# Performance work log

Measured on AMD Instinct MI355X. Metric: run time of the kernel, lower is better.

## Reference

```python
import jax, jax.numpy as jnp
import numpy as np

NEG_SLOPE = 0.01  # torch nn.LeakyReLU default


def setup_inputs() -> dict:
    key = jax.random.key(0)
    ks = jax.random.split(key, 6)
    B, L, C, D = 4, 1024, 128, 64
    return {
        "queries": jax.random.normal(ks[0], (B, L, C), dtype=jnp.float32),
        "keys": jax.random.normal(ks[1], (B, L, C), dtype=jnp.float32),
        "values": jax.random.normal(ks[2], (B, L, C), dtype=jnp.float32),
        "linear_l": jax.random.normal(ks[3], (C, D), dtype=jnp.float32) * 0.05,
        "linear_r": jax.random.normal(ks[4], (C, D), dtype=jnp.float32) * 0.05,
        "a": jax.random.normal(ks[5], (D, 1), dtype=jnp.float32) * 0.05,
    }


def reference(queries, keys, values, linear_l, linear_r, a):
    # keys/values are accepted by the torch forward but unused in its math.
    # g_l, g_r: (B, L, D)
    g_l = jnp.einsum('blc,cd->bld', queries, linear_l)
    g_r = jnp.einsum('blc,cd->bld', queries, linear_r)
    # torch repeat/repeat_interleave + view(b,l,l,-1) yields
    # g_sum[b, x, y] = g_l[b, y] + g_r[b, x]  -> (B, L, L, D)
    g_sum = g_l[:, None, :, :] + g_r[:, :, None, :]
    g_sum = jnp.where(g_sum >= 0, g_sum, NEG_SLOPE * g_sum)  # LeakyReLU
    e = jnp.einsum('bxyd,d->bxy', g_sum, a[:, 0])            # (B, L, L)
    scores = jax.nn.softmax(e, axis=-1)                       # dropout is identity in eval
    y = jnp.einsum('bxy,byd->bxd', scores, g_r)               # (B, L, D)
    return (y, scores)
```

## Files before the change

kernel.cpp:

```cpp
#include <hip/hip_runtime.h>
#include <math.h>

#define LL   1024
#define NROW 4096
#define DD   64
#define CC   128

#define C1H 0.505f
#define C2H 0.495f

typedef short    bf16x8 __attribute__((ext_vector_type(8)));
typedef float    f32x4  __attribute__((ext_vector_type(4)));
typedef _Float16 hf2    __attribute__((ext_vector_type(2)));

#if defined(__has_builtin)
#if __has_builtin(__builtin_amdgcn_fdot2)
#define HAS_FDOT2 1
#endif
#endif

static __device__ __forceinline__ unsigned short bf16rne(float f) {
  unsigned u = __float_as_uint(f);
  u += 0x7fffu + ((u >> 16) & 1u);
  return (unsigned short)(u >> 16);
}

static __device__ __forceinline__ unsigned rflu(unsigned v) {
  return __builtin_amdgcn_readfirstlane(v);
}
static __device__ __forceinline__ float rflf(float v) {
  return __uint_as_float(__builtin_amdgcn_readfirstlane(__float_as_uint(v)));
}

static __device__ __forceinline__ float dot2abs(unsigned glp, unsigned grp,
                                                unsigned ap, float acc) {
  union { unsigned u; hf2 h; } g1, g2, z, av;
  g1.u = glp; g2.u = grp; av.u = ap;
  z.h = g1.h + g2.h;
  z.u &= 0x7fff7fffu;
#ifdef HAS_FDOT2
  return __builtin_amdgcn_fdot2(z.h, av.h, acc, false);
#else
  return fmaf((float)z.h.y, (float)av.h.y,
              fmaf((float)z.h.x, (float)av.h.x, acc));
#endif
}

__global__ __launch_bounds__(256) void k_proj(
    const float* __restrict__ q, const float* __restrict__ Wl,
    const float* __restrict__ Wr, const float* __restrict__ a,
    uint4* __restrict__ glg, _Float16* __restrict__ gr16,
    unsigned short* __restrict__ grT_bf,
    float* __restrict__ AL, float* __restrict__ AR) {
  const int bl0 = blockIdx.x * 8;
  const int b = bl0 >> 10;
  const int t = threadIdx.x;
  __shared__ __align__(16) float qs[8 * CC];
  __shared__ __align__(16) unsigned short trT[DD][8];
  __shared__ __align__(16) _Float16 trL[8][DD];

  ((float4*)qs)[t] = ((const float4*)(q + (size_t)bl0 * CC))[t];
  __syncthreads();

  const int rr = t >> 6;
  const int d  = t & 63;
  const int r0 = rr * 2, r1 = rr * 2 + 1;
  const float* q0 = qs + r0 * CC;
  const float* q1 = qs + r1 * CC;

  float aL0 = 0, aL1 = 0, aR0 = 0, aR1 = 0;
  float bL0 = 0, bL1 = 0, bR0 = 0, bR1 = 0;
#pragma unroll 8
  for (int c = 0; c < CC; c += 2) {
    float wl0 = Wl[c * DD + d],       wr0 = Wr[c * DD + d];
    float wl1 = Wl[(c + 1) * DD + d], wr1 = Wr[(c + 1) * DD + d];
    aL0 = fmaf(q0[c], wl0, aL0);  bL0 = fmaf(q0[c + 1], wl1, bL0);
    aL1 = fmaf(q1[c], wl0, aL1);  bL1 = fmaf(q1[c + 1], wl1, bL1);
    aR0 = fmaf(q0[c], wr0, aR0);  bR0 = fmaf(q0[c + 1], wr1, bR0);
    aR1 = fmaf(q1[c], wr0, aR1);  bR1 = fmaf(q1[c + 1], wr1, bR1);
  }
  float gL0 = aL0 + bL0, gL1 = aL1 + bL1;
  float gR0 = aR0 + bR0, gR1 = aR1 + bR1;

  trL[r0][d] = (_Float16)gL0;
  trL[r1][d] = (_Float16)gL1;
  gr16[(size_t)(bl0 + r0) * DD + d] = (_Float16)gR0;
  gr16[(size_t)(bl0 + r1) * DD + d] = (_Float16)gR1;
  trT[d][r0] = bf16rne(gR0);
  trT[d][r1] = bf16rne(gR1);

  float av = a[d];
  float vL0 = av * gL0, vL1 = av * gL1, vR0 = av * gR0, vR1 = av * gR1;
#pragma unroll
  for (int off = 1; off < 64; off <<= 1) {
    vL0 += __shfl_xor(vL0, off, 64);
    vL1 += __shfl_xor(vL1, off, 64);
    vR0 += __shfl_xor(vR0, off, 64);
    vR1 += __shfl_xor(vR1, off, 64);
  }
  if (d == 0) {
    AL[bl0 + r0] = vL0; AL[bl0 + r1] = vL1;
    AR[bl0 + r0] = vR0; AR[bl0 + r1] = vR1;
  }
  __syncthreads();
  if (t < 64) {
    *(uint4*)&grT_bf[(((size_t)(b * 64 + t)) << 10) + (bl0 & 1023)] =
        *(const uint4*)&trT[t][0];
  } else if (t < 128) {
    int tt = t - 64;
    int r = tt >> 3, g = tt & 7;
    glg[(((size_t)(b * 8 + g)) << 10) + (bl0 & 1023) + r] =
        *(const uint4*)&trL[r][g * 8];
  }
}

__global__ __launch_bounds__(512, 4) void k_fused(
    const uint4* __restrict__ glg, const _Float16* __restrict__ gr16,
    const unsigned short* __restrict__ grT_bf,
    const float* __restrict__ AL, const float* __restrict__ AR,
    const float* __restrict__ a,
    float* __restrict__ scores, float* __restrict__ yout) {
  const int bl0 = blockIdx.x * 8;
  const int b = bl0 >> 10;
  const int t = threadIdx.x;
  const int w = t >> 6, l = t & 63;

  __shared__ __align__(16) _Float16 grL[8 * DD];
  __shared__ __align__(16) unsigned short eb[8704];
  __shared__ __align__(16) float sPV[8][4][8][17];
  __shared__ __align__(16) float sMx[8][8];
  __shared__ __align__(16) float sSx[8][8];

  uint4 gv[4][2][2];
#pragma unroll
  for (int dblk = 0; dblk < 4; ++dblk)
#pragma unroll
    for (int yc = 0; yc < 2; ++yc)
#pragma unroll
      for (int g2 = 0; g2 < 2; ++g2)
        gv[dblk][yc][g2] =
            glg[(((size_t)(b * 8 + dblk * 2 + g2)) << 10) + yc * 512 + t];

  if (t < 256)
    ((unsigned*)grL)[t] = ((const unsigned*)(gr16 + (size_t)bl0 * DD))[t];

  unsigned sa[32];
#pragma unroll
  for (int k = 0; k < 16; ++k) {
    float4 av = *(const float4*)&a[k * 4];
    union { hf2 h; unsigned u; } u0, u1;
    u0.h.x = (_Float16)av.x; u0.h.y = (_Float16)av.y;
    u1.h.x = (_Float16)av.z; u1.h.y = (_Float16)av.w;
    sa[k * 2]     = rflu(u0.u);
    sa[k * 2 + 1] = rflu(u1.u);
  }

  float pr[8];
#pragma unroll
  for (int x = 0; x < 8; ++x) pr[x] = C1H * rflf(AR[bl0 + x]);

  float alv[2];
  alv[0] = AL[b * LL + t];
  alv[1] = AL[b * LL + 512 + t];

  float pacc[8][2];
#pragma unroll
  for (int x = 0; x < 8; ++x) { pacc[x][0] = 0.f; pacc[x][1] = 0.f; }

  __syncthreads();

#pragma unroll
  for (int dblk = 0; dblk < 4; ++dblk) {
#pragma unroll
    for (int x = 0; x < 8; ++x) {
      uint4 gra = *(const uint4*)&grL[x * DD + dblk * 16];
      uint4 grb = *(const uint4*)&grL[x * DD + dblk * 16 + 8];
#pragma unroll
      for (int yc = 0; yc < 2; ++yc) {
        float s = pacc[x][yc];
        s = dot2abs(gv[dblk][yc][0].x, gra.x, sa[dblk * 8 + 0], s);
        s = dot2abs(gv[dblk][yc][0].y, gra.y, sa[dblk * 8 + 1], s);
        s = dot2abs(gv[dblk][yc][0].z, gra.z, sa[dblk * 8 + 2], s);
        s = dot2abs(gv[dblk][yc][0].w, gra.w, sa[dblk * 8 + 3], s);
        s = dot2abs(gv[dblk][yc][1].x, grb.x, sa[dblk * 8 + 4], s);
        s = dot2abs(gv[dblk][yc][1].y, grb.y, sa[dblk * 8 + 5], s);
        s = dot2abs(gv[dblk][yc][1].z, grb.z, sa[dblk * 8 + 6], s);
        s = dot2abs(gv[dblk][yc][1].w, grb.w, sa[dblk * 8 + 7], s);
        pacc[x][yc] = s;
      }
    }
  }

  float ev[8][2];
#pragma unroll
  for (int x = 0; x < 8; ++x)
#pragma unroll
    for (int yc = 0; yc < 2; ++yc)
      ev[x][yc] = fmaf(C2H, pacc[x][yc], pr[x] + C1H * alv[yc]);

  float lm[8];
#pragma unroll
  for (int x = 0; x < 8; ++x) lm[x] = fmaxf(ev[x][0], ev[x][1]);
#pragma unroll
  for (int off = 1; off < 64; off <<= 1) {
#pragma unroll
    for (int x = 0; x < 8; ++x) lm[x] = fmaxf(lm[x], __shfl_xor(lm[x], off, 64));
  }
  if (l == 0) {
#pragma unroll
    for (int x = 0; x < 8; ++x) sMx[x][w] = lm[x];
  }
  __syncthreads();

  float mfin[8], lsum[8];
#pragma unroll
  for (int x = 0; x < 8; ++x) {
    float4 m0 = *(const float4*)&sMx[x][0];
    float4 m1 = *(const float4*)&sMx[x][4];
    mfin[x] = fmaxf(fmaxf(fmaxf(m0.x, m0.y), fmaxf(m0.z, m0.w)),
                    fmaxf(fmaxf(m1.x, m1.y), fmaxf(m1.z, m1.w)));
  }
#pragma unroll
  for (int x = 0; x < 8; ++x) {
    ev[x][0] = __expf(ev[x][0] - mfin[x]);
    ev[x][1] = __expf(ev[x][1] - mfin[x]);
    lsum[x] = ev[x][0] + ev[x][1];
  }
#pragma unroll
  for (int off = 1; off < 64; off <<= 1) {
#pragma unroll
    for (int x = 0; x < 8; ++x) lsum[x] += __shfl_xor(lsum[x], off, 64);
  }
  if (l == 0) {
#pragma unroll
    for (int x = 0; x < 8; ++x) sSx[x][w] = lsum[x];
  }
  __syncthreads();

  float isv[8];
#pragma unroll
  for (int x = 0; x < 8; ++x) {
    float4 s0 = *(const float4*)&sSx[x][0];
    float4 s1 = *(const float4*)&sSx[x][4];
    isv[x] = 1.0f / (((s0.x + s0.y) + (s0.z + s0.w)) +
                     ((s1.x + s1.y) + (s1.z + s1.w)));
  }

#pragma unroll
  for (int yc = 0; yc < 2; ++yc) {
    int y = yc * 512 + t;
    int kc = y >> 5, k32 = t & 31;
#pragma unroll
    for (int x = 0; x < 8; ++x) {
      float p = ev[x][yc] * isv[x];
      __builtin_nontemporal_store(p, &scores[((size_t)(bl0 + x) << 10) + y]);
      eb[kc * 256 + x * 32 + k32] = bf16rne(p);
    }
  }
  __syncthreads();

  f32x4 acc[4] = {{0.f, 0.f, 0.f, 0.f}, {0.f, 0.f, 0.f, 0.f},
                  {0.f, 0.f, 0.f, 0.f}, {0.f, 0.f, 0.f, 0.f}};
  const int row16 = l & 15, hh = l >> 4;
  const size_t bnBase = ((size_t)b * 64) << 10;
#pragma unroll
  for (int kk = 0; kk < 4; ++kk) {
    int kc = w * 4 + kk;
    bf16x8 af = *(const bf16x8*)&eb[kc * 256 + row16 * 32 + hh * 8];
#pragma unroll
    for (int nt = 0; nt < 4; ++nt) {
      bf16x8 bfv = *(const bf16x8*)(grT_bf + bnBase +
                     (((size_t)(nt * 16 + row16)) << 10) + kc * 32 + hh * 8);
      acc[nt] = __builtin_amdgcn_mfma_f32_16x16x32_bf16(af, bfv, acc[nt], 0, 0, 0);
    }
  }
  if (l < 32) {
#pragma unroll
    for (int nt = 0; nt < 4; ++nt)
#pragma unroll
      for (int i = 0; i < 4; ++i)
        sPV[w][nt][hh * 4 + i][row16] = acc[nt][i];
  }
  __syncthreads();
  {
    int x = t >> 6, dcol = t & 63, nt = dcol >> 4, col = dcol & 15;
    float r = 0.f;
#pragma unroll
    for (int ww = 0; ww < 8; ++ww) r += sPV[ww][nt][x][col];
    yout[(size_t)(bl0 + x) * DD + dcol] = r;
  }
}

extern "C" void kernel_launch(void* const* d_in, const int* in_sizes, int n_in,
                              void* d_out, int out_size, void* d_ws, size_t ws_size,
                              hipStream_t stream) {
  const float* q  = (const float*)d_in[0];
  const float* Wl = (const float*)d_in[3];
  const float* Wr = (const float*)d_in[4];
  const float* a  = (const float*)d_in[5];

  float* yout = (float*)d_out;
  float* esc  = yout + NROW * DD;

  float* ws = (float*)d_ws;
  float* AL = ws;
  float* AR = AL + NROW;
  uint4* glg = (uint4*)(AR + NROW);
  _Float16* gr16 = (_Float16*)(glg + (size_t)NROW * 8);
  unsigned short* grT_bf = (unsigned short*)(gr16 + (size_t)NROW * DD);

  k_proj <<<NROW / 8, 256, 0, stream>>>(q, Wl, Wr, a, glg, gr16, grT_bf, AL, AR);
  k_fused<<<NROW / 8, 512, 0, stream>>>(glg, gr16, grT_bf, AL, AR, a, esc, yout);
}
```

Before: 38.71 us.

## Halve query rows per block and stream key tiles per d-block

Each fused block now handles 4 query rows instead of 8, doubling the grid to 1024 blocks. Key-side gl vectors are loaded per d-block inside the loop rather than all up front, cutting register pressure, and launch bounds now ask for 8 blocks per CU. The bf16 score tile is padded with zeros so the 16-row MFMA tile still works with 4 valid rows. The aim is more parallelism and occupancy. The cost is twice as many reloads of the key-side data and of grT per query row, and half of each MFMA tile's rows are wasted.

```diff
diff --git a/kernel.cpp b/kernel.cpp
--- a/kernel.cpp
+++ b/kernel.cpp
@@ -114,35 +114,29 @@
   }
 }
 
-__global__ __launch_bounds__(512, 4) void k_fused(
+__global__ __launch_bounds__(512, 8) void k_fused(
     const uint4* __restrict__ glg, const _Float16* __restrict__ gr16,
     const unsigned short* __restrict__ grT_bf,
     const float* __restrict__ AL, const float* __restrict__ AR,
     const float* __restrict__ a,
     float* __restrict__ scores, float* __restrict__ yout) {
-  const int bl0 = blockIdx.x * 8;
+  const int bl0 = blockIdx.x * 4;
   const int b = bl0 >> 10;
   const int t = threadIdx.x;
   const int w = t >> 6, l = t & 63;
 
-  __shared__ __align__(16) _Float16 grL[8 * DD];
-  __shared__ __align__(16) unsigned short eb[8704];
-  __shared__ __align__(16) float sPV[8][4][8][17];
-  __shared__ __align__(16) float sMx[8][8];
-  __shared__ __align__(16) float sSx[8][8];
-
-  uint4 gv[4][2][2];
-#pragma unroll
-  for (int dblk = 0; dblk < 4; ++dblk)
-#pragma unroll
-    for (int yc = 0; yc < 2; ++yc)
-#pragma unroll
-      for (int g2 = 0; g2 < 2; ++g2)
-        gv[dblk][yc][g2] =
-            glg[(((size_t)(b * 8 + dblk * 2 + g2)) << 10) + yc * 512 + t];
-
-  if (t < 256)
+  __shared__ __align__(16) _Float16 grL[4 * DD];
+  __shared__ __align__(16) unsigned short eb[4608];
+  __shared__ __align__(16) float sPV[8][4][4][17];
+  __shared__ __align__(16) float sMx[4][8];
+  __shared__ __align__(16) float sSx[4][8];
+
+  if (t < 128)
     ((unsigned*)grL)[t] = ((const unsigned*)(gr16 + (size_t)bl0 * DD))[t];
+  if (t >= 256 && t < 384) {
+    uint2 z = {0u, 0u};
+    ((uint2*)&eb[4096])[t - 256] = z;
+  }
 
   unsigned sa[32];
 #pragma unroll
@@ -155,73 +149,80 @@
     sa[k * 2 + 1] = rflu(u1.u);
   }
 
-  float pr[8];
-#pragma unroll
-  for (int x = 0; x < 8; ++x) pr[x] = C1H * rflf(AR[bl0 + x]);
+  float pr[4];
+#pragma unroll
+  for (int x = 0; x < 4; ++x) pr[x] = C1H * rflf(AR[bl0 + x]);
 
   float alv[2];
   alv[0] = AL[b * LL + t];
   alv[1] = AL[b * LL + 512 + t];
 
-  float pacc[8][2];
-#pragma unroll
-  for (int x = 0; x < 8; ++x) { pacc[x][0] = 0.f; pacc[x][1] = 0.f; }
+  float pacc[4][2];
+#pragma unroll
+  for (int x = 0; x < 4; ++x) { pacc[x][0] = 0.f; pacc[x][1] = 0.f; }
 
   __syncthreads();
 
 #pragma unroll
   for (int dblk = 0; dblk < 4; ++dblk) {
-#pragma unroll
-    for (int x = 0; x < 8; ++x) {
+    uint4 gv[2][2];
+#pragma unroll
+    for (int yc = 0; yc < 2; ++yc)
+#pragma unroll
+      for (int g2 = 0; g2 < 2; ++g2)
+        gv[yc][g2] =
+            glg[(((size_t)(b * 8 + dblk * 2 + g2)) << 10) + yc * 512 + t];
+#pragma unroll
+    for (int x = 0; x < 4; ++x) {
       uint4 gra = *(const uint4*)&grL[x * DD + dblk * 16];
       uint4 grb = *(const uint4*)&grL[x * DD + dblk * 16 + 8];
 #pragma unroll
       for (int yc = 0; yc < 2; ++yc) {
         float s = pacc[x][yc];
-        s = dot2abs(gv[dblk][yc][0].x, gra.x, sa[dblk * 8 + 0], s);
-        s = dot2abs(gv[dblk][yc][0].y, gra.y, sa[dblk * 8 + 1], s);
-        s = dot2abs(gv[dblk][yc][0].z, gra.z, sa[dblk * 8 + 2], s);
-        s = dot2abs(gv[dblk][yc][0].w, gra.w, sa[dblk * 8 + 3], s);
-        s = dot2abs(gv[dblk][yc][1].x, grb.x, sa[dblk * 8 + 4], s);
-        s = dot2abs(gv[dblk][yc][1].y, grb.y, sa[dblk * 8 + 5], s);
-        s = dot2abs(gv[dblk][yc][1].z, grb.z, sa[dblk * 8 + 6], s);
-        s = dot2abs(gv[dblk][yc][1].w, grb.w, sa[dblk * 8 + 7], s);
+        s = dot2abs(gv[yc][0].x, gra.x, sa[dblk * 8 + 0], s);
+        s = dot2abs(gv[yc][0].y, gra.y, sa[dblk * 8 + 1], s);
+        s = dot2abs(gv[yc][0].z, gra.z, sa[dblk * 8 + 2], s);
+        s = dot2abs(gv[yc][0].w, gra.w, sa[dblk * 8 + 3], s);
+        s = dot2abs(gv[yc][1].x, grb.x, sa[dblk * 8 + 4], s);
+        s = dot2abs(gv[yc][1].y, grb.y, sa[dblk * 8 + 5], s);
+        s = dot2abs(gv[yc][1].z, grb.z, sa[dblk * 8 + 6], s);
+        s = dot2abs(gv[yc][1].w, grb.w, sa[dblk * 8 + 7], s);
         pacc[x][yc] = s;
       }
     }
   }
 
-  float ev[8][2];
-#pragma unroll
-  for (int x = 0; x < 8; ++x)
+  float ev[4][2];
+#pragma unroll
+  for (int x = 0; x < 4; ++x)
 #pragma unroll
     for (int yc = 0; yc < 2; ++yc)
       ev[x][yc] = fmaf(C2H, pacc[x][yc], pr[x] + C1H * alv[yc]);
 
-  float lm[8];
-#pragma unroll
-  for (int x = 0; x < 8; ++x) lm[x] = fmaxf(ev[x][0], ev[x][1]);
+  float lm[4];
+#pragma unroll
+  for (int x = 0; x < 4; ++x) lm[x] = fmaxf(ev[x][0], ev[x][1]);
 #pragma unroll
   for (int off = 1; off < 64; off <<= 1) {
 #pragma unroll
-    for (int x = 0; x < 8; ++x) lm[x] = fmaxf(lm[x], __shfl_xor(lm[x], off, 64));
+    for (int x = 0; x < 4; ++x) lm[x] = fmaxf(lm[x], __shfl_xor(lm[x], off, 64));
   }
   if (l == 0) {
 #pragma unroll
-    for (int x = 0; x < 8; ++x) sMx[x][w] = lm[x];
-  }
-  __syncthreads();
-
-  float mfin[8], lsum[8];
-#pragma unroll
-  for (int x = 0; x < 8; ++x) {
+    for (int x = 0; x < 4; ++x) sMx[x][w] = lm[x];
+  }
+  __syncthreads();
+
+  float mfin[4], lsum[4];
+#pragma unroll
+  for (int x = 0; x < 4; ++x) {
     float4 m0 = *(const float4*)&sMx[x][0];
     float4 m1 = *(const float4*)&sMx[x][4];
     mfin[x] = fmaxf(fmaxf(fmaxf(m0.x, m0.y), fmaxf(m0.z, m0.w)),
                     fmaxf(fmaxf(m1.x, m1.y), fmaxf(m1.z, m1.w)));
   }
 #pragma unroll
-  for (int x = 0; x < 8; ++x) {
+  for (int x = 0; x < 4; ++x) {
     ev[x][0] = __expf(ev[x][0] - mfin[x]);
     ev[x][1] = __expf(ev[x][1] - mfin[x]);
     lsum[x] = ev[x][0] + ev[x][1];
@@ -229,17 +230,17 @@
 #pragma unroll
   for (int off = 1; off < 64; off <<= 1) {
 #pragma unroll
-    for (int x = 0; x < 8; ++x) lsum[x] += __shfl_xor(lsum[x], off, 64);
+    for (int x = 0; x < 4; ++x) lsum[x] += __shfl_xor(lsum[x], off, 64);
   }
   if (l == 0) {
 #pragma unroll
-    for (int x = 0; x < 8; ++x) sSx[x][w] = lsum[x];
-  }
-  __syncthreads();
-
-  float isv[8];
-#pragma unroll
-  for (int x = 0; x < 8; ++x) {
+    for (int x = 0; x < 4; ++x) sSx[x][w] = lsum[x];
+  }
+  __syncthreads();
+
+  float isv[4];
+#pragma unroll
+  for (int x = 0; x < 4; ++x) {
     float4 s0 = *(const float4*)&sSx[x][0];
     float4 s1 = *(const float4*)&sSx[x][4];
     isv[x] = 1.0f / (((s0.x + s0.y) + (s0.z + s0.w)) +
@@ -251,10 +252,10 @@
     int y = yc * 512 + t;
     int kc = y >> 5, k32 = t & 31;
 #pragma unroll
-    for (int x = 0; x < 8; ++x) {
+    for (int x = 0; x < 4; ++x) {
       float p = ev[x][yc] * isv[x];
       __builtin_nontemporal_store(p, &scores[((size_t)(bl0 + x) << 10) + y]);
-      eb[kc * 256 + x * 32 + k32] = bf16rne(p);
+      eb[kc * 128 + x * 32 + k32] = bf16rne(p);
     }
   }
   __syncthreads();
@@ -266,7 +267,7 @@
 #pragma unroll
   for (int kk = 0; kk < 4; ++kk) {
     int kc = w * 4 + kk;
-    bf16x8 af = *(const bf16x8*)&eb[kc * 256 + row16 * 32 + hh * 8];
+    bf16x8 af = *(const bf16x8*)&eb[kc * 128 + row16 * 32 + hh * 8];
 #pragma unroll
     for (int nt = 0; nt < 4; ++nt) {
       bf16x8 bfv = *(const bf16x8*)(grT_bf + bnBase +
@@ -274,15 +275,15 @@
       acc[nt] = __builtin_amdgcn_mfma_f32_16x16x32_bf16(af, bfv, acc[nt], 0, 0, 0);
     }
   }
-  if (l < 32) {
+  if (l < 16) {
 #pragma unroll
     for (int nt = 0; nt < 4; ++nt)
 #pragma unroll
       for (int i = 0; i < 4; ++i)
-        sPV[w][nt][hh * 4 + i][row16] = acc[nt][i];
-  }
-  __syncthreads();
-  {
+        sPV[w][nt][i][l] = acc[nt][i];
+  }
+  __syncthreads();
+  if (t < 256) {
     int x = t >> 6, dcol = t & 63, nt = dcol >> 4, col = dcol & 15;
     float r = 0.f;
 #pragma unroll
@@ -310,5 +311,5 @@
   unsigned short* grT_bf = (unsigned short*)(gr16 + (size_t)NROW * DD);
 
   k_proj <<<NROW / 8, 256, 0, stream>>>(q, Wl, Wr, a, glg, gr16, grT_bf, AL, AR);
-  k_fused<<<NROW / 8, 512, 0, stream>>>(glg, gr16, grT_bf, AL, AR, a, esc, yout);
-}
+  k_fused<<<NROW / 4, 512, 0, stream>>>(glg, gr16, grT_bf, AL, AR, a, esc, yout);
+}
```

After: 44.15 us. 1.14x slower.
